# Kernel tuning notes

Measured on AMD Instinct MI355X. Metric: run time of the kernel, lower is better.

## Reference

```python
import jax, jax.numpy as jnp
import numpy as np
from jax import lax

DIM = 1024
NUM_HEADS = 16
B, L = 4, 4096


def setup_inputs() -> dict:
    key = jax.random.key(0)
    ks = jax.random.split(key, 7)
    D = DIM // NUM_HEADS
    s = lambda fan_in: 1.0 / np.sqrt(fan_in)
    x = jax.random.normal(ks[0], (B, L, DIM), dtype=jnp.float32)
    w_qk = jax.random.uniform(ks[1], (2 * DIM, DIM), jnp.float32, -s(DIM), s(DIM))
    b_qk = jax.random.uniform(ks[2], (2 * DIM,), jnp.float32, -s(DIM), s(DIM))
    w_v = jax.random.uniform(ks[3], (DIM, DIM), jnp.float32, -s(DIM), s(DIM))
    b_v = jax.random.uniform(ks[4], (DIM,), jnp.float32, -s(DIM), s(DIM))
    # depthwise Conv1d: out_channels=D, in_channels/groups=1, kernel=3
    w_lepe = jax.random.uniform(ks[5], (D, 1, 3), jnp.float32, -s(3), s(3))
    b_lepe = jax.random.uniform(ks[6], (D,), jnp.float32, -s(3), s(3))
    return {"x": x, "w_qk": w_qk, "b_qk": b_qk, "w_v": w_v, "b_v": b_v,
            "w_lepe": w_lepe, "b_lepe": b_lepe, "num_heads": NUM_HEADS}


def _lepe_add(a, w_lepe, b_lepe):
    # a: (B,H,L,D). Faithful to torch: raw reshape (NOT transpose) to (B*H, D, L),
    # depthwise conv over last axis, reshape back to (B,H,D,L), then transpose.
    Bc, H, Lc, D = a.shape
    ar = a.reshape(Bc * H, D, Lc)
    conv = lax.conv_general_dilated(
        ar, w_lepe, window_strides=(1,), padding=((1, 1),),
        feature_group_count=D,
        dimension_numbers=("NCH", "OIH", "NCH"))
    conv = conv + b_lepe[None, :, None]
    return a + conv.reshape(Bc, H, D, Lc).transpose(0, 1, 3, 2)


def reference(x, w_qk, b_qk, w_v, b_v, w_lepe, b_lepe, num_heads):
    Bc, Lc, C = x.shape
    H = num_heads
    D = C // H
    qk = (x @ w_qk.T + b_qk).reshape(Bc, Lc, 2, H, D).transpose(2, 0, 3, 1, 4)
    q, k = qk[0], qk[1]                                  # (B,H,L,D)
    v = (x @ w_v.T + b_v).reshape(Bc, Lc, H, D).transpose(0, 2, 1, 3)
    q = jax.nn.elu(q) + 1.0
    k = jax.nn.elu(k) + 1.0
    q = _lepe_add(q, w_lepe, b_lepe)
    k = _lepe_add(k, w_lepe, b_lepe)
    k_mean = k.mean(axis=2, keepdims=True)               # (B,H,1,D)
    z = 1.0 / (jnp.einsum("bhld,bhmd->bhlm", q, k_mean) + 1e-6)  # (B,H,L,1)
    kv = jnp.einsum("bhld,bhle->bhde", k, v) / Lc        # (B,H,D,D)
    out = jnp.einsum("bhld,bhde->bhle", q, kv) * z       # (B,H,L,D)
    return out.transpose(0, 2, 1, 3).reshape(Bc, Lc, C)
```

## Files before the change

kernel.cpp:

```cpp
#include <hip/hip_runtime.h>
#include <hip/hip_bf16.h>
#include <stdint.h>

typedef __bf16 bf16;
typedef __bf16 bf16x8 __attribute__((ext_vector_type(8)));
typedef __bf16 bf16x4 __attribute__((ext_vector_type(4)));
typedef float  f32x4  __attribute__((ext_vector_type(4)));

static __device__ __forceinline__ void gll16(const void* g, void* l) {
    __builtin_amdgcn_global_load_lds((__attribute__((address_space(1))) void*)(void*)g,
                                     (__attribute__((address_space(3))) void*)l, 16, 0, 0);
}

__global__ __launch_bounds__(256) void cvt_f32_bf16(const float* __restrict__ in,
                                                    bf16* __restrict__ out, int n4) {
    int i = blockIdx.x * 256 + threadIdx.x;
    const int stride = gridDim.x * 256;
    for (; i < n4; i += stride) {
        f32x4 v = *(const f32x4*)(in + (size_t)i * 4);
        bf16x4 o;
        o[0] = (bf16)v[0]; o[1] = (bf16)v[1]; o[2] = (bf16)v[2]; o[3] = (bf16)v[3];
        *(bf16x4*)(out + (size_t)i * 4) = o;
    }
}

__global__ __launch_bounds__(256) void gemm_qkv(const bf16* __restrict__ X,
                                                const bf16* __restrict__ W,
                                                const float* __restrict__ b_qk,
                                                const float* __restrict__ b_v,
                                                bf16* __restrict__ Y) {
    __shared__ bf16 sm[8192];
    const int t    = threadIdx.x;
    const int lane = t & 63;
    const int wv   = t >> 6;
    const int wr   = wv >> 1, wc = wv & 1;
    const int m0   = blockIdx.x * 128;
    const int n0   = blockIdx.y * 128;

    const int sr = t >> 2;
    const int sc = (t & 3) * 8;
    const bf16* gA0 = X + (size_t)(m0 + sr) * 1024 + sc;
    const bf16* gA1 = gA0 + (size_t)64 * 1024;
    const bf16* gB0 = W + (size_t)(n0 + sr) * 1024 + sc;
    const bf16* gB1 = gB0 + (size_t)64 * 1024;
    char* smb = (char*)sm;
    char* lA0 = smb + t * 16;
    char* lA1 = smb + 4096  + t * 16;
    char* lB0 = smb + 8192  + t * 16;
    char* lB1 = smb + 12288 + t * 16;

    const bf16* As = sm;
    const bf16* Bs = sm + 4096;
    const int fr = lane & 15;
    const int fk = (lane >> 4) * 8;

    f32x4 acc[4][4] = {};

    for (int k0 = 0; k0 < 1024; k0 += 32) {
        gll16(gA0 + k0, lA0);
        gll16(gA1 + k0, lA1);
        gll16(gB0 + k0, lB0);
        gll16(gB1 + k0, lB1);
        __syncthreads();
        bf16x8 aF[4], bF[4];
#pragma unroll
        for (int mi = 0; mi < 4; ++mi)
            aF[mi] = *(const bf16x8*)(As + (wr * 64 + mi * 16 + fr) * 32 + fk);
#pragma unroll
        for (int ni = 0; ni < 4; ++ni)
            bF[ni] = *(const bf16x8*)(Bs + (wc * 64 + ni * 16 + fr) * 32 + fk);
#pragma unroll
        for (int mi = 0; mi < 4; ++mi)
#pragma unroll
            for (int ni = 0; ni < 4; ++ni)
                acc[mi][ni] = __builtin_amdgcn_mfma_f32_16x16x32_bf16(aF[mi], bF[ni], acc[mi][ni], 0, 0, 0);
        __syncthreads();
    }

    const bool isqk = (n0 < 2048);
#pragma unroll
    for (int ni = 0; ni < 4; ++ni) {
        const int col = n0 + wc * 64 + ni * 16 + (lane & 15);
        const float bv = isqk ? b_qk[col] : b_v[col - 2048];
#pragma unroll
        for (int mi = 0; mi < 4; ++mi) {
            const int row0 = m0 + wr * 64 + mi * 16 + (lane >> 4) * 4;
#pragma unroll
            for (int j = 0; j < 4; ++j) {
                float vo = acc[mi][ni][j] + bv;
                if (isqk) vo = vo > 0.f ? vo + 1.f : expf(vo);
                Y[(size_t)(row0 + j) * 3072 + col] = (bf16)vo;
            }
        }
    }
}

__global__ __launch_bounds__(256) void lepe(const bf16* __restrict__ Y,
                                            const float* __restrict__ wl,
                                            const float* __restrict__ bl,
                                            bf16* __restrict__ qf,
                                            bf16* __restrict__ kf) {
    const int bx = blockIdx.x;
    const int bh = bx >> 6, m = bx & 63;
    const int b = bh >> 4, h = bh & 15;
    const int isK = blockIdx.y;
    const bf16* slab = Y + (size_t)(b * 4096) * 3072 + isK * 1024 + h * 64;
    bf16* outp = (isK ? kf : qf) + (size_t)(b * 4096) * 1024 + h * 64;

    __shared__ bf16  Gs[64][72];
    __shared__ float Cs[64][65];
    __shared__ float ep[64], en[64];
    const int t = threadIdx.x;
    {
        const int d = t >> 2, c0 = (t & 3) * 16;
        const bf16* src = slab + (size_t)(d * 64 + m) * 3072 + c0;
        *(bf16x8*)&Gs[d][c0]     = *(const bf16x8*)src;
        *(bf16x8*)&Gs[d][c0 + 8] = *(const bf16x8*)(src + 8);
    }
    if (t < 64) {
        const int d = t;
        ep[d] = (m > 0)  ? (float)slab[(size_t)(d * 64 + m - 1) * 3072 + 63] : 0.f;
        en[d] = (m < 63) ? (float)slab[(size_t)(d * 64 + m + 1) * 3072 + 0]  : 0.f;
    }
    __syncthreads();
    {
        const int d = t >> 2, j0 = (t & 3) * 16;
        const float w0 = wl[d * 3], w1 = wl[d * 3 + 1], w2 = wl[d * 3 + 2], bb = bl[d];
#pragma unroll
        for (int jj = 0; jj < 16; ++jj) {
            const int j = j0 + jj;
            const float left  = (j == 0)  ? ep[d] : (float)Gs[d][j - 1];
            const float mid   = (float)Gs[d][j];
            const float right = (j == 63) ? en[d] : (float)Gs[d][j + 1];
            Cs[d][j] = w0 * left + w1 * mid + w2 * right + bb;
        }
    }
    __syncthreads();
    {
        const int j = t >> 2, c0 = (t & 3) * 16;
        const size_t l = (size_t)(m * 64 + j);
        const bf16* arow = slab + l * 3072 + c0;
        bf16* orow = outp + l * 1024 + c0;
        bf16x8 a0 = *(const bf16x8*)arow;
        bf16x8 a1 = *(const bf16x8*)(arow + 8);
        bf16x8 o0, o1;
#pragma unroll
        for (int i = 0; i < 8; ++i) {
            o0[i] = (bf16)((float)a0[i] + Cs[c0 + i][j]);
            o1[i] = (bf16)((float)a1[i] + Cs[c0 + 8 + i][j]);
        }
        *(bf16x8*)orow = o0;
        *(bf16x8*)(orow + 8) = o1;
    }
}

__global__ __launch_bounds__(256) void kv_partial(const bf16* __restrict__ kf,
                                                  const bf16* __restrict__ Y,
                                                  float* __restrict__ kvp,
                                                  float* __restrict__ ksp) {
    const int bh = blockIdx.x, ch = blockIdx.y;
    const int b = bh >> 4, h = bh & 15;
    const bf16* K = kf + (size_t)(b * 4096) * 1024 + h * 64;
    const bf16* V = Y + (size_t)(b * 4096) * 3072 + 2048 + h * 64;

    __shared__ float SM[64 * 68 * 2 + 4 * 64];
#define KS(r, c) SM[(r) * 68 + (c)]
#define VS(r, c) SM[4352 + (r) * 68 + (c)]
    float* ksr = SM + 8704;

    const int t = threadIdx.x;
    const int lane = t & 63;
    const int w = t >> 6;
    const int dg = lane >> 3, eg = lane & 7;

    f32x4 acc[8][2] = {};
    f32x4 ks0 = {}, ks1 = {};

    const int j = t >> 2, c0 = (t & 3) * 16;
    const int l0 = ch * 1024;
    const bf16* Kp = K + (size_t)(l0 + j) * 1024 + c0;
    const bf16* Vp = V + (size_t)(l0 + j) * 3072 + c0;
    bf16x8 k0 = *(const bf16x8*)Kp, k1 = *(const bf16x8*)(Kp + 8);
    bf16x8 v0 = *(const bf16x8*)Vp, v1 = *(const bf16x8*)(Vp + 8);

    for (int s = 0; s < 16; ++s) {
        __syncthreads();
        {
            f32x4 a, bx, c, d2;
#pragma unroll
            for (int i = 0; i < 4; ++i) { a[i] = (float)k0[i]; bx[i] = (float)k0[4 + i]; }
            *(f32x4*)&KS(j, c0) = a;  *(f32x4*)&KS(j, c0 + 4) = bx;
#pragma unroll
            for (int i = 0; i < 4; ++i) { c[i] = (float)k1[i]; d2[i] = (float)k1[4 + i]; }
            *(f32x4*)&KS(j, c0 + 8) = c; *(f32x4*)&KS(j, c0 + 12) = d2;
#pragma unroll
            for (int i = 0; i < 4; ++i) { a[i] = (float)v0[i]; bx[i] = (float)v0[4 + i]; }
            *(f32x4*)&VS(j, c0) = a;  *(f32x4*)&VS(j, c0 + 4) = bx;
#pragma unroll
            for (int i = 0; i < 4; ++i) { c[i] = (float)v1[i]; d2[i] = (float)v1[4 + i]; }
            *(f32x4*)&VS(j, c0 + 8) = c; *(f32x4*)&VS(j, c0 + 12) = d2;
        }
        __syncthreads();
        if (s < 15) {
            Kp += (size_t)64 * 1024; Vp += (size_t)64 * 3072;
            k0 = *(const bf16x8*)Kp; k1 = *(const bf16x8*)(Kp + 8);
            v0 = *(const bf16x8*)Vp; v1 = *(const bf16x8*)(Vp + 8);
        }
#pragma unroll
        for (int jj = 0; jj < 16; ++jj) {
            const int l = w * 16 + jj;
            f32x4 ka = *(const f32x4*)&KS(l, dg * 8);
            f32x4 kb = *(const f32x4*)&KS(l, dg * 8 + 4);
            f32x4 va = *(const f32x4*)&VS(l, eg * 8);
            f32x4 vb = *(const f32x4*)&VS(l, eg * 8 + 4);
            ks0 += ka; ks1 += kb;
#pragma unroll
            for (int i = 0; i < 4; ++i) {
                acc[i][0] += ka[i] * va;     acc[i][1] += ka[i] * vb;
                acc[4 + i][0] += kb[i] * va; acc[4 + i][1] += kb[i] * vb;
            }
        }
    }

    __syncthreads();
    if (eg == 0) {
#pragma unroll
        for (int i = 0; i < 4; ++i) {
            ksr[w * 64 + dg * 8 + i]     = ks0[i];
            ksr[w * 64 + dg * 8 + 4 + i] = ks1[i];
        }
    }
    if (w == 1 || w == 3) {
        float* buf = SM + (w >> 1) * 4352 + lane * 68;
#pragma unroll
        for (int i = 0; i < 8; ++i) {
            *(f32x4*)(buf + i * 8) = acc[i][0];
            *(f32x4*)(buf + i * 8 + 4) = acc[i][1];
        }
    }
    __syncthreads();
    if (w == 0 || w == 2) {
        float* buf = SM + (w >> 1) * 4352 + lane * 68;
#pragma unroll
        for (int i = 0; i < 8; ++i) {
            acc[i][0] += *(const f32x4*)(buf + i * 8);
            acc[i][1] += *(const f32x4*)(buf + i * 8 + 4);
        }
    }
    __syncthreads();
    if (w == 2) {
        float* buf = SM + lane * 68;
#pragma unroll
        for (int i = 0; i < 8; ++i) {
            *(f32x4*)(buf + i * 8) = acc[i][0];
            *(f32x4*)(buf + i * 8 + 4) = acc[i][1];
        }
    }
    __syncthreads();
    if (w == 0) {
        float* buf = SM + lane * 68;
#pragma unroll
        for (int i = 0; i < 8; ++i) {
            acc[i][0] += *(const f32x4*)(buf + i * 8);
            acc[i][1] += *(const f32x4*)(buf + i * 8 + 4);
        }
        float* o = kvp + (((size_t)ch * 64 + bh) * 64 + dg * 8) * 64 + eg * 8;
#pragma unroll
        for (int i = 0; i < 8; ++i) {
            *(f32x4*)(o + (size_t)i * 64)     = acc[i][0];
            *(f32x4*)(o + (size_t)i * 64 + 4) = acc[i][1];
        }
        if (eg == 0) {
#pragma unroll
            for (int i = 0; i < 8; ++i) {
                const int d = dg * 8 + i;
                ksp[(size_t)ch * 4096 + bh * 64 + d] =
                    ksr[d] + ksr[64 + d] + ksr[128 + d] + ksr[192 + d];
            }
        }
    }
#undef KS
#undef VS
}

__global__ __launch_bounds__(256) void out_kernel(const bf16* __restrict__ qf,
                                                  const float* __restrict__ kvp,
                                                  const float* __restrict__ ksp,
                                                  float* __restrict__ out) {
    const int bh = blockIdx.x;
    const int b = bh >> 4, h = bh & 15;
    __shared__ float kvS[4096];
    __shared__ float ksS[64];
    const int t = threadIdx.x;
    const float* kp = kvp + (size_t)bh * 4096;
#pragma unroll
    for (int i = 0; i < 4; ++i) {
        const int idx = i * 1024 + t * 4;
        f32x4 v = *(const f32x4*)(kp + idx);
        v = v + *(const f32x4*)(kp + 262144 + idx);
        v = v + *(const f32x4*)(kp + 524288 + idx);
        v = v + *(const f32x4*)(kp + 786432 + idx);
        *(f32x4*)(kvS + idx) = v;
    }
    if (t < 64) {
        ksS[t] = ksp[bh * 64 + t] + ksp[4096 + bh * 64 + t] +
                 ksp[8192 + bh * 64 + t] + ksp[12288 + bh * 64 + t];
    }
    __syncthreads();

    const int rg = t >> 2, eg = t & 3, e0 = eg * 16;
    const int r0 = blockIdx.y * 256 + rg * 4;
    const bf16* qbase = qf + (size_t)(b * 4096 + r0) * 1024 + h * 64;

    bf16x8 qv[4][8];
#pragma unroll
    for (int i = 0; i < 4; ++i)
#pragma unroll
        for (int s = 0; s < 8; ++s)
            qv[i][s] = *(const bf16x8*)(qbase + (size_t)i * 1024 + s * 8);

    float inv[4];
#pragma unroll
    for (int i = 0; i < 4; ++i) {
        float s = 0.f;
#pragma unroll
        for (int ss = 0; ss < 8; ++ss)
#pragma unroll
            for (int jj = 0; jj < 8; ++jj)
                s += (float)qv[i][ss][jj] * ksS[ss * 8 + jj];
        inv[i] = 1.0f / (s + 0.004096f);
    }

    f32x4 acc[4][4] = {};
#pragma unroll
    for (int d = 0; d < 64; ++d) {
        const float* kr = kvS + d * 64 + e0;
        f32x4 k0 = *(const f32x4*)kr;
        f32x4 k1 = *(const f32x4*)(kr + 4);
        f32x4 k2 = *(const f32x4*)(kr + 8);
        f32x4 k3 = *(const f32x4*)(kr + 12);
#pragma unroll
        for (int i = 0; i < 4; ++i) {
            const float qd = (float)qv[i][d >> 3][d & 7];
            acc[i][0] += qd * k0;
            acc[i][1] += qd * k1;
            acc[i][2] += qd * k2;
            acc[i][3] += qd * k3;
        }
    }
#pragma unroll
    for (int i = 0; i < 4; ++i) {
        float* orow = out + (size_t)(b * 4096 + r0 + i) * 1024 + h * 64 + e0;
#pragma unroll
        for (int q = 0; q < 4; ++q)
            *(f32x4*)(orow + q * 4) = acc[i][q] * inv[i];
    }
}

extern "C" void kernel_launch(void* const* d_in, const int* in_sizes, int n_in,
                              void* d_out, int out_size, void* d_ws, size_t ws_size,
                              hipStream_t stream) {
    const float* x      = (const float*)d_in[0];
    const float* w_qk   = (const float*)d_in[1];
    const float* b_qk   = (const float*)d_in[2];
    const float* w_v    = (const float*)d_in[3];
    const float* b_v    = (const float*)d_in[4];
    const float* w_lepe = (const float*)d_in[5];
    const float* b_lepe = (const float*)d_in[6];

    char* ws = (char*)d_ws;
    bf16*  Y   = (bf16*)ws;
    bf16*  xb  = (bf16*)(ws + 100663296);
    bf16*  Wb  = (bf16*)(ws + 134217728);
    float* kvp = (float*)(ws + 167772160);
    float* ksp = (float*)(ws + 171966464);
    bf16* qf = xb;
    bf16* kf = Wb;

    cvt_f32_bf16<<<2048, 256, 0, stream>>>(x, xb, 16777216 / 4);
    cvt_f32_bf16<<<512,  256, 0, stream>>>(w_qk, Wb, 2097152 / 4);
    cvt_f32_bf16<<<256,  256, 0, stream>>>(w_v, Wb + 2097152, 1048576 / 4);
    gemm_qkv<<<dim3(128, 24), 256, 0, stream>>>(xb, Wb, b_qk, b_v, Y);
    lepe<<<dim3(4096, 2), 256, 0, stream>>>(Y, w_lepe, b_lepe, qf, kf);
    kv_partial<<<dim3(64, 4), 256, 0, stream>>>(kf, Y, kvp, ksp);
    out_kernel<<<dim3(64, 16), 256, 0, stream>>>(qf, kvp, ksp, (float*)d_out);
}
```

Measured before the change: 423.5 us.

## Rewrite QKV GEMM with 256x256 tiles, double-buffered LDS pipeline and swizzle

Replaces the 128x128, 256-thread QKV GEMM with a 256x256 tile using 512 threads and BK=64. Global-to-LDS loads for the next k-step are double-buffered and interleaved with MFMA work through explicit vmcnt waits and barriers. LDS is XOR-swizzled to avoid bank conflicts, MFMA sections are raised with setprio, and the block index is remapped for cache locality. The aim is to hide load latency and raise data reuse per LDS byte. In exchange the kernel needs 128 KB of LDS and more registers, which limits occupancy, and the hand-placed waits are easy to get wrong.

```diff
diff --git a/kernel.cpp b/kernel.cpp
--- a/kernel.cpp
+++ b/kernel.cpp
@@ -24,76 +24,116 @@
     }
 }
 
-__global__ __launch_bounds__(256) void gemm_qkv(const bf16* __restrict__ X,
-                                                const bf16* __restrict__ W,
-                                                const float* __restrict__ b_qk,
-                                                const float* __restrict__ b_v,
-                                                bf16* __restrict__ Y) {
-    __shared__ bf16 sm[8192];
+#define WAITV(n) asm volatile("s_waitcnt vmcnt(" #n ")" ::: "memory")
+#define STA(s_, half, pass, k0_) \
+    gll16(Xs + (size_t)((half) * 128 + (pass) * 64) * 1024 + (k0_), \
+          lds + (s_) * 32768 + (half) * 16384 + (pass) * 8192 + t * 16)
+#define STB(s_, half, pass, k0_) \
+    gll16(Ws + (size_t)((half) * 128 + (pass) * 64) * 1024 + (k0_), \
+          lds + 65536 + (s_) * 32768 + (half) * 16384 + (pass) * 8192 + t * 16)
+
+__global__ __launch_bounds__(512, 2) void gemm_qkv(const bf16* __restrict__ X,
+                                                   const bf16* __restrict__ W,
+                                                   const float* __restrict__ b_qk,
+                                                   const float* __restrict__ b_v,
+                                                   bf16* __restrict__ Y) {
+    __shared__ char lds[131072];
     const int t    = threadIdx.x;
     const int lane = t & 63;
-    const int wv   = t >> 6;
-    const int wr   = wv >> 1, wc = wv & 1;
-    const int m0   = blockIdx.x * 128;
-    const int n0   = blockIdx.y * 128;
-
-    const int sr = t >> 2;
-    const int sc = (t & 3) * 8;
-    const bf16* gA0 = X + (size_t)(m0 + sr) * 1024 + sc;
-    const bf16* gA1 = gA0 + (size_t)64 * 1024;
-    const bf16* gB0 = W + (size_t)(n0 + sr) * 1024 + sc;
-    const bf16* gB1 = gB0 + (size_t)64 * 1024;
-    char* smb = (char*)sm;
-    char* lA0 = smb + t * 16;
-    char* lA1 = smb + 4096  + t * 16;
-    char* lB0 = smb + 8192  + t * 16;
-    char* lB1 = smb + 12288 + t * 16;
-
-    const bf16* As = sm;
-    const bf16* Bs = sm + 4096;
+    const int wid  = t >> 6;
+    const int wm   = wid >> 2, wn = wid & 3;
+
+    const int bid = blockIdx.x;
+    const int wg  = (bid & 7) * 96 + (bid >> 3);
+    const int m0  = (wg & 63) * 256;
+    const int n0  = (wg >> 6) * 256;
+
+    const int scol = (((t & 7) ^ ((t >> 3) & 7)) * 8);
+    const bf16* Xs = X + (size_t)(m0 + (t >> 3)) * 1024 + scol;
+    const bf16* Ws = W + (size_t)(n0 + (t >> 3)) * 1024 + scol;
+
     const int fr = lane & 15;
-    const int fk = (lane >> 4) * 8;
-
-    f32x4 acc[4][4] = {};
-
-    for (int k0 = 0; k0 < 1024; k0 += 32) {
-        gll16(gA0 + k0, lA0);
-        gll16(gA1 + k0, lA1);
-        gll16(gB0 + k0, lB0);
-        gll16(gB1 + k0, lB1);
-        __syncthreads();
-        bf16x8 aF[4], bF[4];
-#pragma unroll
-        for (int mi = 0; mi < 4; ++mi)
-            aF[mi] = *(const bf16x8*)(As + (wr * 64 + mi * 16 + fr) * 32 + fk);
-#pragma unroll
-        for (int ni = 0; ni < 4; ++ni)
-            bF[ni] = *(const bf16x8*)(Bs + (wc * 64 + ni * 16 + fr) * 32 + fk);
-#pragma unroll
-        for (int mi = 0; mi < 4; ++mi)
-#pragma unroll
-            for (int ni = 0; ni < 4; ++ni)
-                acc[mi][ni] = __builtin_amdgcn_mfma_f32_16x16x32_bf16(aF[mi], bF[ni], acc[mi][ni], 0, 0, 0);
-        __syncthreads();
+    const int l7 = lane & 7;
+    const int ax0 = (((lane >> 4) + 0) ^ l7) << 4;
+    const int ax1 = (((lane >> 4) + 4) ^ l7) << 4;
+    const int baseA = wm * 16384 + fr * 128;
+    const int baseB = 65536 + (wn >> 1) * 16384 + ((wn & 1) * 64 + fr) * 128;
+
+    f32x4 acc[8][4] = {};
+    bf16x8 bF[4][2];
+
+    STB(0, 0, 0, 0); STB(0, 0, 1, 0); STB(0, 1, 0, 0); STB(0, 1, 1, 0);
+    STA(0, 0, 0, 0); STA(0, 1, 0, 0); STA(0, 0, 1, 0); STA(0, 1, 1, 0);
+    WAITV(2);
+    __builtin_amdgcn_s_barrier();
+
+    for (int j = 0; j < 16; ++j) {
+        const int s  = j & 1;
+        const int sn = s ^ 1;
+        const int kn = (j + 1) << 6;
+        const bool st = j < 15;
+        const int sA = s * 32768 + baseA;
+        const int sB = s * 32768 + baseB;
+
+#pragma unroll
+        for (int q = 0; q < 4; ++q) {
+            bf16x8 aF[2][2];
+#pragma unroll
+            for (int m2 = 0; m2 < 2; ++m2) {
+                aF[m2][0] = *(const bf16x8*)(lds + sA + (q * 2 + m2) * 2048 + ax0);
+                aF[m2][1] = *(const bf16x8*)(lds + sA + (q * 2 + m2) * 2048 + ax1);
+            }
+            if (q == 0) {
+#pragma unroll
+                for (int nf = 0; nf < 4; ++nf) {
+                    bF[nf][0] = *(const bf16x8*)(lds + sB + nf * 2048 + ax0);
+                    bF[nf][1] = *(const bf16x8*)(lds + sB + nf * 2048 + ax1);
+                }
+            }
+            if (st) {
+                if      (q == 0) { STB(sn, 0, 0, kn); STB(sn, 0, 1, kn); }
+                else if (q == 1) { STB(sn, 1, 0, kn); STB(sn, 1, 1, kn); }
+                else if (q == 2) { STA(sn, 0, 0, kn); STA(sn, 1, 0, kn); }
+                else             { STA(sn, 0, 1, kn); STA(sn, 1, 1, kn); }
+            }
+            __builtin_amdgcn_s_barrier();
+            __builtin_amdgcn_s_setprio(1);
+#pragma unroll
+            for (int m2 = 0; m2 < 2; ++m2)
+#pragma unroll
+                for (int nf = 0; nf < 4; ++nf)
+#pragma unroll
+                    for (int kk = 0; kk < 2; ++kk)
+                        acc[q * 2 + m2][nf] = __builtin_amdgcn_mfma_f32_16x16x32_bf16(
+                            aF[m2][kk], bF[nf][kk], acc[q * 2 + m2][nf], 0, 0, 0);
+            __builtin_amdgcn_s_setprio(0);
+            if (q == 1) { if (st) { WAITV(4); } else { WAITV(0); } }
+            if (q == 3 && st) { WAITV(2); }
+            __builtin_amdgcn_s_barrier();
+        }
     }
 
     const bool isqk = (n0 < 2048);
-#pragma unroll
-    for (int ni = 0; ni < 4; ++ni) {
-        const int col = n0 + wc * 64 + ni * 16 + (lane & 15);
+    const int crow = (lane >> 4) * 4;
+#pragma unroll
+    for (int nf = 0; nf < 4; ++nf) {
+        const int col = n0 + wn * 64 + nf * 16 + (lane & 15);
         const float bv = isqk ? b_qk[col] : b_v[col - 2048];
 #pragma unroll
-        for (int mi = 0; mi < 4; ++mi) {
-            const int row0 = m0 + wr * 64 + mi * 16 + (lane >> 4) * 4;
-#pragma unroll
-            for (int j = 0; j < 4; ++j) {
-                float vo = acc[mi][ni][j] + bv;
+        for (int mf = 0; mf < 8; ++mf) {
+            const int row0 = m0 + wm * 128 + mf * 16 + crow;
+#pragma unroll
+            for (int jj = 0; jj < 4; ++jj) {
+                float vo = acc[mf][nf][jj] + bv;
                 if (isqk) vo = vo > 0.f ? vo + 1.f : expf(vo);
-                Y[(size_t)(row0 + j) * 3072 + col] = (bf16)vo;
-            }
-        }
-    }
-}
+                Y[(size_t)(row0 + jj) * 3072 + col] = (bf16)vo;
+            }
+        }
+    }
+}
+#undef STA
+#undef STB
+#undef WAITV
 
 __global__ __launch_bounds__(256) void lepe(const bf16* __restrict__ Y,
                                             const float* __restrict__ wl,
@@ -380,7 +420,7 @@
     cvt_f32_bf16<<<2048, 256, 0, stream>>>(x, xb, 16777216 / 4);
     cvt_f32_bf16<<<512,  256, 0, stream>>>(w_qk, Wb, 2097152 / 4);
     cvt_f32_bf16<<<256,  256, 0, stream>>>(w_v, Wb + 2097152, 1048576 / 4);
-    gemm_qkv<<<dim3(128, 24), 256, 0, stream>>>(xb, Wb, b_qk, b_v, Y);
+    gemm_qkv<<<768, 512, 0, stream>>>(xb, Wb, b_qk, b_v, Y);
     lepe<<<dim3(4096, 2), 256, 0, stream>>>(Y, w_lepe, b_lepe, qf, kf);
     kv_partial<<<dim3(64, 4), 256, 0, stream>>>(kf, Y, kvp, ksp);
     out_kernel<<<dim3(64, 16), 256, 0, stream>>>(qf, kvp, ksp, (float*)d_out);
```

After: 414.3 us. -2.2%, faster.
